# Optimization experiments

Hardware: AMD Instinct MI355X
Metric: run time of the kernel (lower is better)

The kernel has to match this reference:

```python
import jax, jax.numpy as jnp
import numpy as np

B, C_IN, N, K, UP = 4, 128, 1024, 9, 4
EPS_BN = 1e-5


def _grid():
    # gen_grid(4): num_x=num_y=2, linspace(-0.2,0.2,2) -> (4,2)
    g = jnp.linspace(-0.2, 0.2, 2)
    x, y = jnp.meshgrid(g, g, indexing='ij')
    return jnp.stack([x, y], axis=-1).reshape(-1, 2)


def _knn(x, k, dilation):
    # x: (B,C,N). L2-normalize features, matrix pairwise dist, top-k, dilated select.
    nrm = jnp.sqrt(jnp.sum(x * x, axis=1, keepdims=True))
    xn = x / jnp.maximum(nrm, 1e-12)
    xt = xn.transpose(0, 2, 1)                      # (B,N,C)
    sq = jnp.sum(xt * xt, axis=-1)                  # (B,N)
    dist = sq[:, :, None] - 2.0 * jnp.einsum('bnc,bmc->bnm', xt, xt) + sq[:, None, :]
    _, idx = jax.lax.top_k(-dist, k * dilation)     # k*d nearest (incl. self)
    return idx[:, :, ::dilation]                    # (B,N,k)


def _bn(x, g, b, axes):
    # training-mode batchnorm over given axes, channel axis = 1
    m = jnp.mean(x, axis=axes, keepdims=True)
    v = jnp.mean((x - m) ** 2, axis=axes, keepdims=True)
    sh = [1] * x.ndim
    sh[1] = -1
    return (x - m) * jax.lax.rsqrt(v + EPS_BN) * g.reshape(sh) + b.reshape(sh)


def _edge_conv(x, k, dil, W, g, b):
    # DGCNN edge conv: gather neighbors, [x_i, x_j-x_i], 1x1 conv, BN, relu, max over k
    idx = _knn(x, k, dil)                                        # (B,N,k)
    x_j = jax.vmap(lambda xx, ii: xx[:, ii])(x, idx)             # (B,C,N,k)
    x_i = jnp.broadcast_to(x[..., None], x_j.shape)
    feat = jnp.concatenate([x_i, x_j - x_i], axis=1)             # (B,2C,N,k)
    out = jnp.einsum('oc,bcnk->bonk', W, feat)
    out = jax.nn.relu(_bn(out, g, b, (0, 2, 3)))
    return jnp.max(out, axis=-1)                                 # (B,Cout,N)


def _conv1d(x, W, b):
    return jnp.einsum('oc,bcn->bon', W, x) + b[None, :, None]


def _atten(x, Wf, bf, gf, bef, Wg, bg, gg, beg, Wh, bh, gh, beh, gamma):
    # attention_unit / RA_Layer1 math (C=130)
    f = jax.nn.relu(_bn(_conv1d(x, Wf, bf), gf, bef, (0, 2)))    # (B,C/4,M)
    g_ = jax.nn.relu(_bn(_conv1d(x, Wg, bg), gg, beg, (0, 2)))
    h = jax.nn.relu(_bn(_conv1d(x, Wh, bh), gh, beh, (0, 2)))    # (B,C,M)
    s = jnp.einsum('bcn,bcm->bnm', g_, f)                        # g^T @ f: (B,M,M)
    beta = jax.nn.softmax(s, axis=2)
    o = jnp.einsum('bcn,bnm->bcm', h, beta)                      # h @ beta
    return gamma * o + x


def _forward(inp, Wa, gna, bta, Wb, gnb, btb, Wf, bf, gf, bef, Wg, bg, gg, beg,
             Wh, bh, gh, beh, gamma, W1, b1, W2, b2):
    x1 = _edge_conv(inp, K, 1, Wa, gna, bta)                     # (B,256,N)
    x2 = _edge_conv(inp, K, 2, Wb, gnb, btb)                     # (B,256,N)
    x = jnp.concatenate([x1, x2], axis=1)                        # (B,512,N)
    net = x.transpose(0, 2, 1).reshape(B, N * UP, 128)           # (B,4N,128)
    grid = jnp.repeat(_grid(), N, axis=0)                        # (4N,2)
    grid = jnp.broadcast_to(grid[None], (B, N * UP, 2)).astype(net.dtype)
    net = jnp.concatenate([net, grid], axis=2).transpose(0, 2, 1)  # (B,130,4N)
    net = _atten(net, Wf, bf, gf, bef, Wg, bg, gg, beg, Wh, bh, gh, beh, gamma)
    net = jax.nn.relu(_conv1d(net, W1, b1))                      # 130->256
    net = jax.nn.relu(_conv1d(net, W2, b2))                      # 256->128
    return net                                                   # (B,128,4N)


def setup_inputs() -> dict:
    key = jax.random.key(0)
    ks = jax.random.split(key, 24)
    rn = lambda k, sh, s=0.05: jax.random.normal(k, sh, jnp.float32) * s
    d = {
        'inp': jax.random.normal(ks[0], (B, C_IN, N), jnp.float32),
        'Wa': rn(ks[1], (256, 256)), 'gna': 1.0 + rn(ks[2], (256,)), 'bta': rn(ks[3], (256,)),
        'Wb': rn(ks[4], (256, 256)), 'gnb': 1.0 + rn(ks[5], (256,)), 'btb': rn(ks[6], (256,)),
        'Wf': rn(ks[7], (32, 130)), 'bf': rn(ks[8], (32,)), 'gf': 1.0 + rn(ks[9], (32,)), 'bef': rn(ks[9], (32,)),
        'Wg': rn(ks[10], (32, 130)), 'bg': rn(ks[11], (32,)), 'gg': 1.0 + rn(ks[12], (32,)), 'beg': rn(ks[12], (32,)),
        'Wh': rn(ks[13], (130, 130)), 'bh': rn(ks[14], (130,)), 'gh': 1.0 + rn(ks[15], (130,)), 'beh': rn(ks[15], (130,)),
        'gamma': rn(ks[16], (), 1.0),
        'W1': rn(ks[17], (256, 130)), 'b1': rn(ks[18], (256,)),
        'W2': rn(ks[19], (128, 256)), 'b2': rn(ks[20], (128,)),
    }
    return d


def reference(inp, Wa, gna, bta, Wb, gnb, btb, Wf, bf, gf, bef, Wg, bg, gg, beg,
              Wh, bh, gh, beh, gamma, W1, b1, W2, b2):
    return _forward(inp, Wa, gna, bta, Wb, gnb, btb, Wf, bf, gf, bef, Wg, bg, gg, beg,
                    Wh, bh, gh, beh, gamma, W1, b1, W2, b2)
```

## Files before the change

kernel.cpp:

```cpp
#include <hip/hip_runtime.h>

namespace {
constexpr int NB = 4;
constexpr int CI = 128;
constexpr int NP = 1024;
constexpr int MM = 4096;
constexpr float EPSBN = 1e-5f;
constexpr float LOG2E = 1.4426950408889634f;

constexpr size_t OPS_SH = 2162688;
constexpr size_t OFF_OP   = 0;
constexpr size_t OFF_DIST = 0;
constexpr size_t OFF_PM   = 0;
constexpr size_t OFF_QM   = 2097152;
constexpr size_t OFF_HRAW = 0;
constexpr size_t OFF_FGRAW= 2359296;
constexpr size_t OFF_Y1   = 0;
constexpr size_t OFF_FGT  = 6488064;
constexpr size_t OFF_HB   = 7012352;
constexpr size_t OFF_A16  = 6488064;
constexpr size_t OFF_X16  = 8192000;
constexpr size_t OFF_LSE  = 9502720;
constexpr size_t OFF_LSEP = 9519104;
constexpr size_t OFF_STATS= 9650176;
constexpr size_t OFF_ABE  = 9715712;
constexpr size_t OFF_ABFG = 9716736;
constexpr size_t OFF_ABH  = 9716864;
constexpr size_t OFF_FGP  = 9717376;
constexpr size_t OFF_BIAS = 9725568;
constexpr size_t OFF_W16  = 9726208;
constexpr size_t OFF_KNN  = 9779712;
constexpr size_t OFF_XN   = 9853440;
constexpr size_t OFF_SQ   = 10377728;
constexpr size_t OFF_XR   = 10381824;
constexpr size_t OFF_WPQ  = 10643968;
constexpr size_t W16_FG = 0;
constexpr size_t W16_H  = 10240;
constexpr size_t W16_C1 = 33280;
constexpr size_t W16_C2 = 74240;
constexpr size_t B_FG = 0, B_H = 64, B_C1 = 208, B_C2 = 464;
}

typedef __attribute__((ext_vector_type(8))) short short8;
typedef __attribute__((ext_vector_type(4))) float f32x4;
#define MFMA16(A, B, C) __builtin_amdgcn_mfma_f32_16x16x32_bf16(A, B, C, 0, 0, 0)

__device__ inline unsigned short f2bf(float x) {
  unsigned int u = __float_as_uint(x);
  unsigned int r = u + 0x7fff + ((u >> 16) & 1);
  return (unsigned short)(r >> 16);
}
__device__ inline float bf2f(unsigned short s) {
  return __uint_as_float(((unsigned int)s) << 16);
}
__device__ inline unsigned cvtpk(float lo, float hi) {
  unsigned r;
  asm("v_cvt_pk_bf16_f32 %0, %1, %2" : "=v"(r) : "v"(lo), "v"(hi));
  return r;
}

__global__ __launch_bounds__(256) void k_prep(const float* __restrict__ Wf, const float* __restrict__ Wg,
                                              const float* __restrict__ Wh, const float* __restrict__ W1,
                                              const float* __restrict__ W2, const float* __restrict__ bf,
                                              const float* __restrict__ bg, const float* __restrict__ bh,
                                              const float* __restrict__ b1, const float* __restrict__ b2,
                                              unsigned short* __restrict__ W16, float* __restrict__ BIAS) {
  int i = blockIdx.x * 256 + threadIdx.x;
  if (i < 107008) {
    float v = 0.f;
    if (i < 10240) { int o = i / 160, c = i % 160; if (c < 130) v = (o < 32) ? Wf[o * 130 + c] : Wg[(o - 32) * 130 + c]; }
    else if (i < 33280) { int r = i - 10240; int o = r / 160, c = r % 160; if (o < 130 && c < 130) v = Wh[o * 130 + c]; }
    else if (i < 74240) { int r = i - 33280; int o = r / 160, c = r % 160; if (c < 130) v = W1[o * 130 + c]; }
    else { int r = i - 74240; int o = r / 256, c = r % 256; v = W2[o * 256 + c]; }
    W16[i] = f2bf(v);
  } else if (i < 107648) {
    int j = i - 107008; float v = 0.f;
    if (j < 64) v = (j < 32) ? bf[j] : bg[j - 32];
    else if (j < 208) { int c = j - 64; if (c < 130) v = bh[c]; }
    else if (j < 464) v = b1[j - 208];
    else if (j < 592) v = b2[j - 464];
    BIAS[j] = v;
  }
}

__global__ __launch_bounds__(256) void k_prep2(const float* __restrict__ Wa, const float* __restrict__ Wb,
                                               unsigned short* __restrict__ WPQ) {
  int i = blockIdx.x * 256 + threadIdx.x;
  int e = i >> 16;
  int rem = i & 65535;
  int pq = rem >> 15;
  int rr = rem & 32767;
  int o = rr >> 7, c = rr & 127;
  const float* W = e ? Wb : Wa;
  float w1 = W[o * 256 + c], w2 = W[o * 256 + 128 + c];
  float v = pq ? w2 : (w1 - w2);
  WPQ[i] = f2bf(v);
}

__global__ __launch_bounds__(256) void k_norm(const float* __restrict__ x,
                                              float* __restrict__ xn,
                                              unsigned short* __restrict__ XR,
                                              float* __restrict__ sq) {
  int t = blockIdx.x * 256 + threadIdx.x;
  int b = t >> 10, n = t & 1023;
  const float* xb = x + (size_t)b * CI * NP + n;
  float ss = 0.f;
  #pragma unroll 4
  for (int c = 0; c < CI; ++c) { float v = xb[(size_t)c * NP]; ss += v * v; }
  float inv = 1.f / fmaxf(sqrtf(ss), 1e-12f);
  float* xo = xn + (size_t)b * CI * NP + n;
  float s2 = 0.f;
  for (int c0 = 0; c0 < 128; c0 += 8) {
    unsigned rw[4];
    #pragma unroll
    for (int j = 0; j < 4; ++j) {
      float va = xb[(size_t)(c0 + 2 * j) * NP];
      float vb = xb[(size_t)(c0 + 2 * j + 1) * NP];
      float na = va * inv, nb = vb * inv;
      s2 += na * na + nb * nb;
      xo[(size_t)(c0 + 2 * j) * NP] = na;
      xo[(size_t)(c0 + 2 * j + 1) * NP] = nb;
      rw[j] = (unsigned)f2bf(va) | ((unsigned)f2bf(vb) << 16);
    }
    uint4 r4 = {rw[0], rw[1], rw[2], rw[3]};
    *(uint4*)&XR[(size_t)t * 128 + c0] = r4;
  }
  sq[t] = s2;
}

__global__ __launch_bounds__(256) void k_dist(const float* __restrict__ xn,
                                              const float* __restrict__ sq,
                                              float* __restrict__ dist) {
  __shared__ float As[32][68], Bs[32][68];
  int t = threadIdx.x;
  int m0 = blockIdx.x * 64, n0 = blockIdx.y * 64, b = blockIdx.z;
  int mg = t & 15, ng = t >> 4;
  float acc[16];
  #pragma unroll
  for (int i = 0; i < 16; ++i) acc[i] = 0.f;
  for (int cc = 0; cc < 128; cc += 32) {
    __syncthreads();
    for (int idx = t; idx < 2048; idx += 256) {
      int c = idx >> 6, j = idx & 63;
      As[c][j] = xn[((size_t)b * CI + cc + c) * NP + n0 + j];
      Bs[c][j] = xn[((size_t)b * CI + cc + c) * NP + m0 + j];
    }
    __syncthreads();
    #pragma unroll
    for (int c = 0; c < 32; ++c) {
      float4 avv = *(const float4*)&As[c][ng * 4];
      float4 bvv = *(const float4*)&Bs[c][mg * 4];
      float a[4] = {avv.x, avv.y, avv.z, avv.w};
      float bb[4] = {bvv.x, bvv.y, bvv.z, bvv.w};
      #pragma unroll
      for (int i = 0; i < 4; ++i)
        #pragma unroll
        for (int j = 0; j < 4; ++j) acc[i * 4 + j] += a[i] * bb[j];
    }
  }
  #pragma unroll
  for (int i = 0; i < 4; ++i) {
    int n = n0 + ng * 4 + i;
    float sn = sq[b * NP + n];
    float4 r;
    r.x = sn + sq[b * NP + m0 + mg * 4 + 0] - 2.f * acc[i * 4 + 0];
    r.y = sn + sq[b * NP + m0 + mg * 4 + 1] - 2.f * acc[i * 4 + 1];
    r.z = sn + sq[b * NP + m0 + mg * 4 + 2] - 2.f * acc[i * 4 + 2];
    r.w = sn + sq[b * NP + m0 + mg * 4 + 3] - 2.f * acc[i * 4 + 3];
    *(float4*)&dist[((size_t)b * NP + n) * NP + m0 + mg * 4] = r;
  }
}

__global__ __launch_bounds__(64) void k_knn(const float* __restrict__ dist,
                                            int* __restrict__ knn) {
  int row = blockIdx.x;
  int l = threadIdx.x;
  const float* dr = dist + (size_t)row * NP;
  float d[16];
  #pragma unroll
  for (int i = 0; i < 16; ++i) d[i] = dr[l + 64 * i];
  for (int s = 0; s < 18; ++s) {
    float best = __builtin_inff(); int bslot = -1;
    #pragma unroll
    for (int i = 0; i < 16; ++i) if (d[i] < best) { best = d[i]; bslot = i; }
    int bidx = (bslot >= 0) ? (l + 64 * bslot) : 0x7fffffff;
    float bd = best; int bi = bidx;
    #pragma unroll
    for (int off = 32; off > 0; off >>= 1) {
      float od = __shfl_xor(bd, off);
      int   oi = __shfl_xor(bi, off);
      if (od < bd || (od == bd && oi < bi)) { bd = od; bi = oi; }
    }
    if (l == 0) knn[row * 18 + s] = bi;
    if ((bi & 63) == l) d[bi >> 6] = __builtin_inff();
  }
}

__global__ __launch_bounds__(256) void k_pqm(const unsigned short* __restrict__ XR,
                                             const unsigned short* __restrict__ WPQ,
                                             float* __restrict__ Pm,
                                             float* __restrict__ Qm) {
  int t = threadIdx.x; int w = t >> 6; int l = t & 63;
  int lm = l & 15, g = l >> 4;
  int nt = blockIdx.x, oq = blockIdx.y, z = blockIdx.z;
  int e = z >> 2, b = z & 3;
  int srow = nt * 64 + w * 16 + lm;
  const unsigned short* sp = XR + ((size_t)b * 1024 + srow) * 128 + 8 * g;
  const unsigned short* wpp = WPQ + ((size_t)(e * 2 + 0) * 256 + oq * 64 + lm) * 128 + 8 * g;
  const unsigned short* wqq = WPQ + ((size_t)(e * 2 + 1) * 256 + oq * 64 + lm) * 128 + 8 * g;
  f32x4 accp[4], accq[4];
  #pragma unroll
  for (int i = 0; i < 4; ++i) { accp[i] = {0.f, 0.f, 0.f, 0.f}; accq[i] = {0.f, 0.f, 0.f, 0.f}; }
  #pragma unroll
  for (int cc = 0; cc < 4; ++cc) {
    short8 bfr = *(const short8*)(sp + cc * 32);
    #pragma unroll
    for (int ct = 0; ct < 4; ++ct) {
      short8 ap = *(const short8*)(wpp + (size_t)ct * 16 * 128 + cc * 32);
      accp[ct] = MFMA16(ap, bfr, accp[ct]);
      short8 aq = *(const short8*)(wqq + (size_t)ct * 16 * 128 + cc * 32);
      accq[ct] = MFMA16(aq, bfr, accq[ct]);
    }
  }
  int eb = e * 4 + b;
  #pragma unroll
  for (int ct = 0; ct < 4; ++ct) {
    int o0 = oq * 64 + ct * 16 + 4 * g;
    float4 rp = {accp[ct][0], accp[ct][1], accp[ct][2], accp[ct][3]};
    float4 rq = {accq[ct][0], accq[ct][1], accq[ct][2], accq[ct][3]};
    *(float4*)&Pm[((size_t)eb * 1024 + srow) * 256 + o0] = rp;
    *(float4*)&Qm[((size_t)eb * 1024 + srow) * 256 + o0] = rq;
  }
}

__global__ __launch_bounds__(256) void k_edge_stats(const float* __restrict__ Pm,
                                                    const float* __restrict__ Qm,
                                                    const int* __restrict__ knn,
                                                    float* __restrict__ stats) {
  int o = threadIdx.x;
  int chunk = blockIdx.x, b = blockIdx.y, e = blockIdx.z;
  int eb = e * 4 + b;
  float s = 0.f, s2 = 0.f;
  for (int nn = 0; nn < 64; ++nn) {
    int n = chunk * 64 + nn;
    float p = Pm[((size_t)eb * 1024 + n) * 256 + o];
    const int* kn = knn + (b * 1024 + n) * 18;
    #pragma unroll
    for (int kk = 0; kk < 9; ++kk) {
      int j = kn[e ? 2 * kk : kk];
      float v = p + Qm[((size_t)eb * 1024 + j) * 256 + o];
      s += v; s2 += v * v;
    }
  }
  size_t idx = ((((size_t)e * 4 + b) * 16 + chunk) * 256 + o) * 2;
  stats[idx] = s; stats[idx + 1] = s2;
}

__global__ __launch_bounds__(256) void k_edge_fin(const float* __restrict__ stats,
                                                  const float* __restrict__ gna, const float* __restrict__ bta,
                                                  const float* __restrict__ gnb, const float* __restrict__ btb,
                                                  float* __restrict__ ab) {
  int i = blockIdx.x * 256 + threadIdx.x;
  if (i >= 512) return;
  int e = i >> 8, o = i & 255;
  float s = 0.f, s2 = 0.f;
  for (int b = 0; b < 4; ++b)
    for (int ch = 0; ch < 16; ++ch) {
      size_t idx = ((((size_t)e * 4 + b) * 16 + ch) * 256 + o) * 2;
      s += stats[idx]; s2 += stats[idx + 1];
    }
  float cnt = 4.0f * 1024.0f * 9.0f;
  float mean = s / cnt;
  float var = s2 / cnt - mean * mean;
  float g = e ? gnb[o] : gna[o];
  float bt = e ? btb[o] : bta[o];
  float alpha = g * rsqrtf(var + EPSBN);
  ab[i * 2] = alpha; ab[i * 2 + 1] = bt - mean * alpha;
}

__global__ __launch_bounds__(256) void k_edge_apply(const float* __restrict__ Pm,
                                                    const float* __restrict__ Qm,
                                                    const int* __restrict__ knn,
                                                    const float* __restrict__ ab,
                                                    unsigned short* __restrict__ X16) {
  __shared__ int knl[18];
  int t = threadIdx.x;
  int n = blockIdx.x, b = blockIdx.y;
  if (t < 18) knl[t] = knn[(b * 1024 + n) * 18 + t];
  __syncthreads();
  int e = t >> 7, oo = t & 127;
  int eb = e * 4 + b;
  const float* Pr = Pm + ((size_t)eb * 1024 + n) * 256;
  const float* Qb = Qm + (size_t)eb * 1024 * 256;
  float p0 = Pr[oo], p1 = Pr[oo + 128];
  float a0 = ab[(e * 256 + oo) * 2], be0 = ab[(e * 256 + oo) * 2 + 1];
  float a1 = ab[(e * 256 + oo + 128) * 2], be1 = ab[(e * 256 + oo + 128) * 2 + 1];
  float mx0 = -__builtin_inff(), mx1 = -__builtin_inff();
  #pragma unroll
  for (int kk = 0; kk < 9; ++kk) {
    int j = knl[e ? 2 * kk : kk];
    const float* Qr = Qb + (size_t)j * 256;
    mx0 = fmaxf(mx0, fmaf(a0, p0 + Qr[oo], be0));
    mx1 = fmaxf(mx1, fmaf(a1, p1 + Qr[oo + 128], be1));
  }
  int u0 = e << 1, u1 = (e << 1) | 1;
  X16[((size_t)b * MM + 4 * n + u0) * 160 + oo] = f2bf(fmaxf(mx0, 0.f));
  X16[((size_t)b * MM + 4 * n + u1) * 160 + oo] = f2bf(fmaxf(mx1, 0.f));
  if (t < 128) {
    int u = t >> 5, c = 128 + (t & 31);
    int gr = n >> 8;
    float v = (c == 128) ? ((gr < 2) ? -0.2f : 0.2f) : (c == 129) ? ((gr & 1) ? 0.2f : -0.2f) : 0.f;
    X16[((size_t)b * MM + 4 * n + u) * 160 + c] = f2bf(v);
  }
}

template <int KSTEPS, int CTPER, int OUTMODE, bool RELU>
__global__ __launch_bounds__(256) void k_convm(const unsigned short* __restrict__ src,
                                               const unsigned short* __restrict__ W16,
                                               const float* __restrict__ bias,
                                               float* __restrict__ dstF,
                                               unsigned short* __restrict__ dstB,
                                               int outld, int rows) {
  constexpr int LD = KSTEPS * 32;
  int t = threadIdx.x; int w = t >> 6; int l = t & 63;
  int lm = l & 15, g = l >> 4;
  int b = blockIdx.z; int ct0 = blockIdx.y * CTPER;
  int srow = blockIdx.x * 64 + w * 16 + lm;
  const unsigned short* sp = src + ((size_t)b * MM + srow) * LD + 8 * g;
  const unsigned short* wp = W16 + ((size_t)ct0 * 16 + lm) * LD + 8 * g;
  f32x4 acc[CTPER];
  #pragma unroll
  for (int i = 0; i < CTPER; ++i) acc[i] = {0.f, 0.f, 0.f, 0.f};
  #pragma unroll
  for (int cc = 0; cc < KSTEPS; ++cc) {
    short8 bfr = *(const short8*)(sp + cc * 32);
    #pragma unroll
    for (int ct = 0; ct < CTPER; ++ct) {
      short8 af = *(const short8*)(wp + (size_t)ct * 16 * LD + cc * 32);
      acc[ct] = MFMA16(af, bfr, acc[ct]);
    }
  }
  #pragma unroll
  for (int ct = 0; ct < CTPER; ++ct) {
    int o0 = (ct0 + ct) * 16 + 4 * g;
    float4 bv = *(const float4*)&bias[o0];
    float v[4] = {acc[ct][0] + bv.x, acc[ct][1] + bv.y, acc[ct][2] + bv.z, acc[ct][3] + bv.w};
    if (RELU) { v[0] = fmaxf(v[0], 0.f); v[1] = fmaxf(v[1], 0.f); v[2] = fmaxf(v[2], 0.f); v[3] = fmaxf(v[3], 0.f); }
    if (OUTMODE == 0) {
      float4 r = {v[0], v[1], v[2], v[3]};
      *(float4*)&dstF[((size_t)b * MM + srow) * outld + o0] = r;
    } else if (OUTMODE == 1) {
      uint2 pk;
      pk.x = cvtpk(v[0], v[1]);
      pk.y = cvtpk(v[2], v[3]);
      *(uint2*)&dstB[((size_t)b * MM + srow) * outld + o0] = pk;
    } else {
      #pragma unroll
      for (int r = 0; r < 4; ++r)
        dstF[((size_t)b * rows + o0 + r) * MM + srow] = v[r];
    }
  }
}

__global__ __launch_bounds__(256) void k_fgstats(const float* __restrict__ FGraw,
                                                 float* __restrict__ FGP) {
  __shared__ float red[4][64][2];
  int t = threadIdx.x; int c = t & 63, rq = t >> 6;
  int blk = blockIdx.x;
  float s = 0.f, s2 = 0.f;
  for (int k = 0; k < 64; ++k) {
    int r = blk * 256 + rq + 4 * k;
    float v = FGraw[(size_t)r * 64 + c];
    s += v; s2 += v * v;
  }
  red[rq][c][0] = s; red[rq][c][1] = s2;
  __syncthreads();
  if (t < 64) {
    float a = 0.f, a2 = 0.f;
    #pragma unroll
    for (int q = 0; q < 4; ++q) { a += red[q][t][0]; a2 += red[q][t][1]; }
    FGP[((size_t)blk * 64 + t) * 2] = a; FGP[((size_t)blk * 64 + t) * 2 + 1] = a2;
  }
}

__global__ __launch_bounds__(64) void k_fgfin(const float* __restrict__ FGP,
                                              const float* __restrict__ gf, const float* __restrict__ bef,
                                              const float* __restrict__ gg, const float* __restrict__ beg,
                                              float* __restrict__ ab) {
  int c = threadIdx.x;
  float s = 0.f, s2 = 0.f;
  for (int blk = 0; blk < 64; ++blk) { s += FGP[((size_t)blk * 64 + c) * 2]; s2 += FGP[((size_t)blk * 64 + c) * 2 + 1]; }
  float cnt = 16384.f;
  float mean = s / cnt, var = s2 / cnt - mean * mean;
  float gv = (c < 32) ? gf[c] : gg[c - 32];
  float bv = (c < 32) ? bef[c] : beg[c - 32];
  float alpha = gv * rsqrtf(var + EPSBN);
  ab[c * 2] = alpha; ab[c * 2 + 1] = bv - mean * alpha;
}

__global__ __launch_bounds__(256) void k_bnstats(const float* __restrict__ src,
                                                 const float* __restrict__ g,
                                                 const float* __restrict__ be,
                                                 float* __restrict__ ab, int ldC) {
  int o = blockIdx.x;
  int t = threadIdx.x;
  float s = 0.f, s2 = 0.f;
  for (int b = 0; b < NB; ++b) {
    const float* r = src + ((size_t)b * ldC + o) * MM;
    for (int m = t; m < MM; m += 256) { float v = r[m]; s += v; s2 += v * v; }
  }
  __shared__ float rs[256], rs2[256];
  rs[t] = s; rs2[t] = s2;
  __syncthreads();
  for (int off = 128; off > 0; off >>= 1) {
    if (t < off) { rs[t] += rs[t + off]; rs2[t] += rs2[t + off]; }
    __syncthreads();
  }
  if (t == 0) {
    float cnt = 16384.0f;
    float mean = rs[0] / cnt, var = rs2[0] / cnt - mean * mean;
    float alpha = g[o] * rsqrtf(var + EPSBN);
    ab[o * 2] = alpha; ab[o * 2 + 1] = be[o] - mean * alpha;
  }
}

__global__ __launch_bounds__(256) void k_cvtFG(const float* __restrict__ FGraw,
                                               const float* __restrict__ ab,
                                               unsigned short* __restrict__ FGT) {
  int i = blockIdx.x * 256 + threadIdx.x;
  int row = i >> 3, c0 = (i & 7) * 8;
  float sc = (c0 < 32) ? LOG2E : 1.0f;
  float vv[8];
  float4 u0 = *(const float4*)&FGraw[(size_t)row * 64 + c0];
  float4 u1 = *(const float4*)&FGraw[(size_t)row * 64 + c0 + 4];
  vv[0] = u0.x; vv[1] = u0.y; vv[2] = u0.z; vv[3] = u0.w;
  vv[4] = u1.x; vv[5] = u1.y; vv[6] = u1.z; vv[7] = u1.w;
  uint4 pk;
  unsigned pw[4];
  #pragma unroll
  for (int h = 0; h < 4; ++h) {
    int c = c0 + 2 * h;
    float a0 = ab[c * 2] * sc, b0 = ab[c * 2 + 1] * sc;
    float a1 = ab[(c + 1) * 2] * sc, b1 = ab[(c + 1) * 2 + 1] * sc;
    float x0 = fmaxf(fmaf(a0, vv[2 * h], b0), 0.f);
    float x1 = fmaxf(fmaf(a1, vv[2 * h + 1], b1), 0.f);
    pw[h] = cvtpk(x0, x1);
  }
  pk.x = pw[0]; pk.y = pw[1]; pk.z = pw[2]; pk.w = pw[3];
  *(uint4*)&FGT[(size_t)row * 64 + c0] = pk;
}

__global__ __launch_bounds__(256) void k_cvtH(const float* __restrict__ src,
                                              const float* __restrict__ ab,
                                              unsigned short* __restrict__ dst) {
  int i = blockIdx.x * 256 + threadIdx.x;
  int m4 = i & 1023; int c = (i >> 10) % 144; int b = i / (144 * 1024);
  ushort4 ov = {0, 0, 0, 0};
  if (c < 130) {
    float4 v = *(const float4*)&src[((size_t)b * 144 + c) * MM + m4 * 4];
    float a = ab[c * 2], be = ab[c * 2 + 1];
    ov.x = f2bf(fmaxf(fmaf(a, v.x, be), 0.f));
    ov.y = f2bf(fmaxf(fmaf(a, v.y, be), 0.f));
    ov.z = f2bf(fmaxf(fmaf(a, v.z, be), 0.f));
    ov.w = f2bf(fmaxf(fmaf(a, v.w, be), 0.f));
  }
  *(ushort4*)&dst[((size_t)b * 144 + c) * MM + m4 * 4] = ov;
}

__global__ __launch_bounds__(256) void k_zlse(const unsigned short* __restrict__ FGT,
                                              float* __restrict__ LSEP) {
  int t = threadIdx.x; int w = t >> 6; int l = t & 63;
  int b = blockIdx.z; int ms = blockIdx.y;
  int n0 = blockIdx.x * 64 + w * 16;
  int lm = l & 15, g = l >> 4;
  f32x4 z4 = {0.f, 0.f, 0.f, 0.f};
  short8 af = *(const short8*)&FGT[((size_t)b * MM + n0 + lm) * 64 + 32 + 8 * g];
  float rm[4], zz[4];
  #pragma unroll
  for (int r = 0; r < 4; ++r) { rm[r] = -__builtin_inff(); zz[r] = 0.f; }
  for (int it = 0; it < 16; ++it) {
    int m0 = ms * 1024 + it * 64;
    short8 bfr[4];
    #pragma unroll
    for (int mi = 0; mi < 4; ++mi)
      bfr[mi] = *(const short8*)&FGT[((size_t)b * MM + m0 + mi * 16 + lm) * 64 + 8 * g];
    f32x4 d[4];
    #pragma unroll
    for (int mi = 0; mi < 4; ++mi) d[mi] = MFMA16(af, bfr[mi], z4);
    #pragma unroll
    for (int r = 0; r < 4; ++r) {
      float tm = fmaxf(fmaxf(d[0][r], d[1][r]), fmaxf(d[2][r], d[3][r]));
      float nm = fmaxf(rm[r], tm);
      zz[r] = zz[r] * exp2f(rm[r] - nm)
            + exp2f(d[0][r] - nm) + exp2f(d[1][r] - nm)
            + exp2f(d[2][r] - nm) + exp2f(d[3][r] - nm);
      rm[r] = nm;
    }
  }
  #pragma unroll
  for (int off = 1; off < 16; off <<= 1) {
    #pragma unroll
    for (int r = 0; r < 4; ++r) {
      float om = __shfl_xor(rm[r], off);
      float oz = __shfl_xor(zz[r], off);
      float nm = fmaxf(rm[r], om);
      zz[r] = zz[r] * exp2f(rm[r] - nm) + oz * exp2f(om - nm);
      rm[r] = nm;
    }
  }
  if (lm == 0) {
    #pragma unroll
    for (int r = 0; r < 4; ++r) {
      int n = n0 + 4 * g + r;
      size_t idx = ((size_t)ms * 16384 + (size_t)b * MM + n) * 2;
      LSEP[idx] = rm[r]; LSEP[idx + 1] = zz[r];
    }
  }
}

__global__ __launch_bounds__(256) void k_lsered(const float* __restrict__ LSEP,
                                                float* __restrict__ LSE) {
  int bn = blockIdx.x * 256 + threadIdx.x;
  float rm = -__builtin_inff(), zz = 0.f;
  #pragma unroll
  for (int ms = 0; ms < 4; ++ms) {
    float m = LSEP[((size_t)ms * 16384 + bn) * 2];
    float z = LSEP[((size_t)ms * 16384 + bn) * 2 + 1];
    float nm = fmaxf(rm, m);
    zz = zz * exp2f(rm - nm) + z * exp2f(m - nm);
    rm = nm;
  }
  LSE[bn] = rm + log2f(zz);
}

__global__ __launch_bounds__(256) void k_omfma(const unsigned short* __restrict__ FGT,
                                               const unsigned short* __restrict__ HB,
                                               const float* __restrict__ LSE,
                                               unsigned short* __restrict__ Opart) {
  int t = threadIdx.x; int w = t >> 6; int l = t & 63;
  int b = blockIdx.y; int split = blockIdx.z;
  int lm = l & 15, g = l >> 4;
  int mcol0 = blockIdx.x * 128 + w * 32 + lm;
  int mcol1 = mcol0 + 16;
  f32x4 z4 = {0.f, 0.f, 0.f, 0.f};
  short8 Ff0 = *(const short8*)&FGT[((size_t)b * MM + mcol0) * 64 + 8 * g];
  short8 Ff1 = *(const short8*)&FGT[((size_t)b * MM + mcol1) * 64 + 8 * g];
  f32x4 acc0[9], acc1[9];
  #pragma unroll
  for (int ct = 0; ct < 9; ++ct) { acc0[ct] = z4; acc1[ct] = z4; }
  const int nchunks = (split < 2) ? 22 : 21;
  const int startc = split * 21 + ((split < 2) ? split : 2);
  const int start = startc * 32;
  const int end = start + nchunks * 32;
  const unsigned short* gptr = FGT + ((size_t)b * MM + lm) * 64 + 32 + 8 * g;
  const unsigned short* hbase = HB + ((size_t)b * 144 + lm) * MM + 8 * g;
  const float* lbase = LSE + (size_t)b * MM + 4 * g;
  int src01 = lm + 16 * (2 * (g & 1));
  int src23 = src01 + 16;
  bool hi = g >= 2;

  short8 a0 = *(const short8*)(gptr + (size_t)start * 64);
  short8 a1 = *(const short8*)(gptr + (size_t)(start + 16) * 64);
  float4 l0 = *(const float4*)(lbase + start);
  float4 l1 = *(const float4*)(lbase + start + 16);

  for (int n0 = start; n0 < end; n0 += 32) {
    const unsigned short* hp = hbase + n0;
    short8 hf[9];
    #pragma unroll
    for (int ct = 0; ct < 9; ++ct) hf[ct] = *(const short8*)(hp + (size_t)ct * 16 * MM);
    f32x4 s00 = MFMA16(a0, Ff0, z4);
    f32x4 s10 = MFMA16(a1, Ff0, z4);
    f32x4 s01 = MFMA16(a0, Ff1, z4);
    f32x4 s11 = MFMA16(a1, Ff1, z4);
    int nn = (n0 + 32 < end) ? (n0 + 32) : start;
    short8 na0 = *(const short8*)(gptr + (size_t)nn * 64);
    short8 na1 = *(const short8*)(gptr + (size_t)(nn + 16) * 64);
    float4 nl0 = *(const float4*)(lbase + nn);
    float4 nl1 = *(const float4*)(lbase + nn + 16);
    float le0[4] = {l0.x, l0.y, l0.z, l0.w};
    float le1[4] = {l1.x, l1.y, l1.z, l1.w};
    unsigned pk00[2], pk10[2], pk01[2], pk11[2];
    #pragma unroll
    for (int h2 = 0; h2 < 2; ++h2) {
      float e00a = exp2f(s00[2 * h2] - le0[2 * h2]);
      float e00b = exp2f(s00[2 * h2 + 1] - le0[2 * h2 + 1]);
      float e10a = exp2f(s10[2 * h2] - le1[2 * h2]);
      float e10b = exp2f(s10[2 * h2 + 1] - le1[2 * h2 + 1]);
      float e01a = exp2f(s01[2 * h2] - le0[2 * h2]);
      float e01b = exp2f(s01[2 * h2 + 1] - le0[2 * h2 + 1]);
      float e11a = exp2f(s11[2 * h2] - le1[2 * h2]);
      float e11b = exp2f(s11[2 * h2 + 1] - le1[2 * h2 + 1]);
      pk00[h2] = cvtpk(e00a, e00b);
      pk10[h2] = cvtpk(e10a, e10b);
      pk01[h2] = cvtpk(e01a, e01b);
      pk11[h2] = cvtpk(e11a, e11b);
    }
    a0 = na0; a1 = na1; l0 = nl0; l1 = nl1;
    unsigned a0w = (unsigned)__shfl((int)pk00[0], src01);
    unsigned b0w = (unsigned)__shfl((int)pk10[0], src01);
    unsigned a1w = (unsigned)__shfl((int)pk00[1], src01);
    unsigned b1w = (unsigned)__shfl((int)pk10[1], src01);
    unsigned a2w = (unsigned)__shfl((int)pk00[0], src23);
    unsigned b2w = (unsigned)__shfl((int)pk10[0], src23);
    unsigned a3w = (unsigned)__shfl((int)pk00[1], src23);
    unsigned b3w = (unsigned)__shfl((int)pk10[1], src23);
    union { unsigned u[4]; short8 s; } bu0;
    bu0.u[0] = hi ? b0w : a0w; bu0.u[1] = hi ? b1w : a1w;
    bu0.u[2] = hi ? b2w : a2w; bu0.u[3] = hi ? b3w : a3w;
    short8 bfrag0 = bu0.s;
    unsigned c0w = (unsigned)__shfl((int)pk01[0], src01);
    unsigned d0w = (unsigned)__shfl((int)pk11[0], src01);
    unsigned c1w = (unsigned)__shfl((int)pk01[1], src01);
    unsigned d1w = (unsigned)__shfl((int)pk11[1], src01);
    unsigned c2w = (unsigned)__shfl((int)pk01[0], src23);
    unsigned d2w = (unsigned)__shfl((int)pk11[0], src23);
    unsigned c3w = (unsigned)__shfl((int)pk01[1], src23);
    unsigned d3w = (unsigned)__shfl((int)pk11[1], src23);
    union { unsigned u[4]; short8 s; } bu1;
    bu1.u[0] = hi ? d0w : c0w; bu1.u[1] = hi ? d1w : c1w;
    bu1.u[2] = hi ? d2w : c2w; bu1.u[3] = hi ? d3w : c3w;
    short8 bfrag1 = bu1.s;
    #pragma unroll
    for (int ct = 0; ct < 9; ++ct) {
      acc0[ct] = MFMA16(hf[ct], bfrag0, acc0[ct]);
      acc1[ct] = MFMA16(hf[ct], bfrag1, acc1[ct]);
    }
  }
  unsigned short* op0 = Opart + (size_t)split * OPS_SH + ((size_t)b * MM + mcol0) * 132;
  unsigned short* op1 = Opart + (size_t)split * OPS_SH + ((size_t)b * MM + mcol1) * 132;
  #pragma unroll
  for (int ct = 0; ct < 9; ++ct) {
    int c0 = ct * 16 + 4 * g;
    if (c0 < 132) {
      uint2 p0, p1;
      p0.x = cvtpk(acc0[ct][0], acc0[ct][1]);
      p0.y = cvtpk(acc0[ct][2], acc0[ct][3]);
      p1.x = cvtpk(acc1[ct][0], acc1[ct][1]);
      p1.y = cvtpk(acc1[ct][2], acc1[ct][3]);
      *(uint2*)&op0[c0] = p0;
      *(uint2*)&op1[c0] = p1;
    }
  }
}

__global__ __launch_bounds__(256) void k_ored(const unsigned short* __restrict__ Op,
                                              const unsigned short* __restrict__ X16,
                                              const float* __restrict__ gma,
                                              unsigned short* __restrict__ A16) {
  int i = blockIdx.x * 256 + threadIdx.x;
  int row = i / 20, c8 = i % 20;
  int c0 = c8 * 8;
  unsigned short* ap = A16 + (size_t)row * 160 + c0;
  if (c0 >= 136) {
    uint4 z = {0, 0, 0, 0};
    *(uint4*)ap = z;
    return;
  }
  float gm = gma[0];
  float ov[8] = {0.f, 0.f, 0.f, 0.f, 0.f, 0.f, 0.f, 0.f};
  #pragma unroll
  for (int s = 0; s < 6; ++s) {
    const unsigned short* base = Op + (size_t)s * OPS_SH + (size_t)row * 132 + c0;
    uint2 u = *(const uint2*)base;
    ov[0] += bf2f((unsigned short)(u.x & 0xffff));
    ov[1] += bf2f((unsigned short)(u.x >> 16));
    ov[2] += bf2f((unsigned short)(u.y & 0xffff));
    ov[3] += bf2f((unsigned short)(u.y >> 16));
    if (c0 + 4 < 132) {
      uint2 v = *(const uint2*)(base + 4);
      ov[4] += bf2f((unsigned short)(v.x & 0xffff));
      ov[5] += bf2f((unsigned short)(v.x >> 16));
      ov[6] += bf2f((unsigned short)(v.y & 0xffff));
      ov[7] += bf2f((unsigned short)(v.y >> 16));
    }
  }
  short8 xv = *(const short8*)(X16 + (size_t)row * 160 + c0);
  unsigned pw[4];
  #pragma unroll
  for (int h = 0; h < 4; ++h) {
    int ca = c0 + 2 * h, cb = c0 + 2 * h + 1;
    float xa = bf2f((unsigned short)xv[2 * h]);
    float xb = bf2f((unsigned short)xv[2 * h + 1]);
    float va = (ca < 132) ? (gm * ov[2 * h] + xa) : 0.f;
    float vb = (cb < 132) ? (gm * ov[2 * h + 1] + xb) : 0.f;
    pw[h] = (unsigned)f2bf(va) | ((unsigned)f2bf(vb) << 16);
  }
  uint4 pk = {pw[0], pw[1], pw[2], pw[3]};
  *(uint4*)ap = pk;
}

extern "C" void kernel_launch(void* const* d_in, const int* in_sizes, int n_in,
                              void* d_out, int out_size, void* d_ws, size_t ws_size,
                              hipStream_t stream) {
  const float* inp = (const float*)d_in[0];
  const float* Wa  = (const float*)d_in[1];
  const float* gna = (const float*)d_in[2];
  const float* bta = (const float*)d_in[3];
  const float* Wb  = (const float*)d_in[4];
  const float* gnb = (const float*)d_in[5];
  const float* btb = (const float*)d_in[6];
  const float* Wf  = (const float*)d_in[7];
  const float* bf  = (const float*)d_in[8];
  const float* gf  = (const float*)d_in[9];
  const float* bef = (const float*)d_in[10];
  const float* Wg  = (const float*)d_in[11];
  const float* bg  = (const float*)d_in[12];
  const float* gg  = (const float*)d_in[13];
  const float* beg = (const float*)d_in[14];
  const float* Wh  = (const float*)d_in[15];
  const float* bh  = (const float*)d_in[16];
  const float* gh  = (const float*)d_in[17];
  const float* beh = (const float*)d_in[18];
  const float* gamma = (const float*)d_in[19];
  const float* W1  = (const float*)d_in[20];
  const float* b1  = (const float*)d_in[21];
  const float* W2  = (const float*)d_in[22];
  const float* b2  = (const float*)d_in[23];
  float* out = (float*)d_out;

  float* ws = (float*)d_ws;
  float* DIST = ws + OFF_DIST;
  float* PM   = ws + OFF_PM;
  float* QM   = ws + OFF_QM;
  float* HRAW = ws + OFF_HRAW;
  float* FGRAW= ws + OFF_FGRAW;
  unsigned short* OP16 = (unsigned short*)(ws + OFF_OP);
  unsigned short* FGT = (unsigned short*)(ws + OFF_FGT);
  unsigned short* HBB = (unsigned short*)(ws + OFF_HB);
  unsigned short* A16 = (unsigned short*)(ws + OFF_A16);
  unsigned short* X16 = (unsigned short*)(ws + OFF_X16);
  unsigned short* Y1  = (unsigned short*)(ws + OFF_Y1);
  float* LSEB = ws + OFF_LSE;
  float* LSEP = ws + OFF_LSEP;
  float* STATS= ws + OFF_STATS;
  float* ABE  = ws + OFF_ABE;
  float* ABFG = ws + OFF_ABFG;
  float* ABH  = ws + OFF_ABH;
  float* FGP  = ws + OFF_FGP;
  float* BIAS = ws + OFF_BIAS;
  unsigned short* W16 = (unsigned short*)(ws + OFF_W16);
  int*   KNNI = (int*)(ws + OFF_KNN);
  float* XN   = ws + OFF_XN;
  unsigned short* XR = (unsigned short*)(ws + OFF_XR);
  unsigned short* WPQ = (unsigned short*)(ws + OFF_WPQ);
  float* SQ   = ws + OFF_SQ;

  k_prep<<<421, 256, 0, stream>>>(Wf, Wg, Wh, W1, W2, bf, bg, bh, b1, b2, W16, BIAS);
  k_prep2<<<512, 256, 0, stream>>>(Wa, Wb, WPQ);
  k_norm<<<16, 256, 0, stream>>>(inp, XN, XR, SQ);
  k_dist<<<dim3(16, 16, 4), 256, 0, stream>>>(XN, SQ, DIST);
  k_knn<<<4096, 64, 0, stream>>>(DIST, KNNI);
  k_pqm<<<dim3(16, 4, 8), 256, 0, stream>>>(XR, WPQ, PM, QM);
  k_edge_stats<<<dim3(16, 4, 2), 256, 0, stream>>>(PM, QM, KNNI, STATS);
  k_edge_fin<<<2, 256, 0, stream>>>(STATS, gna, bta, gnb, btb, ABE);
  k_edge_apply<<<dim3(1024, 4), 256, 0, stream>>>(PM, QM, KNNI, ABE, X16);
  k_convm<5, 2, 0, false><<<dim3(64, 2, 4), 256, 0, stream>>>(X16, W16 + W16_FG, BIAS + B_FG, FGRAW, nullptr, 64, 0);
  k_convm<5, 3, 2, false><<<dim3(64, 3, 4), 256, 0, stream>>>(X16, W16 + W16_H, BIAS + B_H, HRAW, nullptr, 0, 144);
  k_fgstats<<<64, 256, 0, stream>>>(FGRAW, FGP);
  k_fgfin<<<1, 64, 0, stream>>>(FGP, gf, bef, gg, beg, ABFG);
  k_bnstats<<<130, 256, 0, stream>>>(HRAW, gh, beh, ABH, 144);
  k_cvtFG<<<512, 256, 0, stream>>>(FGRAW, ABFG, FGT);
  k_cvtH<<<2304, 256, 0, stream>>>(HRAW, ABH, HBB);
  k_zlse<<<dim3(64, 4, 4), 256, 0, stream>>>(FGT, LSEP);
  k_lsered<<<64, 256, 0, stream>>>(LSEP, LSEB);
  k_omfma<<<dim3(32, 4, 6), 256, 0, stream>>>(FGT, HBB, LSEB, OP16);
  k_ored<<<1280, 256, 0, stream>>>(OP16, X16, gamma, A16);
  k_convm<5, 8, 1, true><<<dim3(64, 2, 4), 256, 0, stream>>>(A16, W16 + W16_C1, BIAS + B_C1, nullptr, Y1, 256, 0);
  k_convm<8, 4, 2, true><<<dim3(64, 2, 4), 256, 0, stream>>>(Y1, W16 + W16_C2, BIAS + B_C2, out, nullptr, 0, 128);
}
```

Before: 352.3 us.

## Store raw F/G/H conv outputs in bf16, merge prep kernels, deepen omfma prefetch

The F/G and H 1x1 conv outputs are now written in bf16 rather than fp32. BN statistics and the normalize/ReLU apply step read those bf16 buffers, and H is normalized in place. This halves intermediate memory traffic, at the cost of computing BN statistics on bf16-rounded values. The two weight-prep kernels are merged into one launch. The attention MFMA loop is software-pipelined two iterations ahead so the score MFMAs for the next tile overlap with the current softmax and accumulation.

```diff
diff --git a/kernel.cpp b/kernel.cpp
--- a/kernel.cpp
+++ b/kernel.cpp
@@ -13,8 +13,7 @@
 constexpr size_t OFF_DIST = 0;
 constexpr size_t OFF_PM   = 0;
 constexpr size_t OFF_QM   = 2097152;
-constexpr size_t OFF_HRAW = 0;
-constexpr size_t OFF_FGRAW= 2359296;
+constexpr size_t OFF_FGR  = 2359296;
 constexpr size_t OFF_Y1   = 0;
 constexpr size_t OFF_FGT  = 6488064;
 constexpr size_t OFF_HB   = 7012352;
@@ -64,7 +63,9 @@
                                               const float* __restrict__ W2, const float* __restrict__ bf,
                                               const float* __restrict__ bg, const float* __restrict__ bh,
                                               const float* __restrict__ b1, const float* __restrict__ b2,
-                                              unsigned short* __restrict__ W16, float* __restrict__ BIAS) {
+                                              const float* __restrict__ Wa, const float* __restrict__ Wb,
+                                              unsigned short* __restrict__ W16, float* __restrict__ BIAS,
+                                              unsigned short* __restrict__ WPQ) {
   int i = blockIdx.x * 256 + threadIdx.x;
   if (i < 107008) {
     float v = 0.f;
@@ -80,21 +81,18 @@
     else if (j < 464) v = b1[j - 208];
     else if (j < 592) v = b2[j - 464];
     BIAS[j] = v;
-  }
-}
-
-__global__ __launch_bounds__(256) void k_prep2(const float* __restrict__ Wa, const float* __restrict__ Wb,
-                                               unsigned short* __restrict__ WPQ) {
-  int i = blockIdx.x * 256 + threadIdx.x;
-  int e = i >> 16;
-  int rem = i & 65535;
-  int pq = rem >> 15;
-  int rr = rem & 32767;
-  int o = rr >> 7, c = rr & 127;
-  const float* W = e ? Wb : Wa;
-  float w1 = W[o * 256 + c], w2 = W[o * 256 + 128 + c];
-  float v = pq ? w2 : (w1 - w2);
-  WPQ[i] = f2bf(v);
+  } else if (i < 238720) {
+    int j = i - 107648;
+    int e = j >> 16;
+    int rem = j & 65535;
+    int pq = rem >> 15;
+    int rr = rem & 32767;
+    int o = rr >> 7, c = rr & 127;
+    const float* W = e ? Wb : Wa;
+    float w1 = W[o * 256 + c], w2 = W[o * 256 + 128 + c];
+    float v = pq ? w2 : (w1 - w2);
+    WPQ[j] = f2bf(v);
+  }
 }
 
 __global__ __launch_bounds__(256) void k_norm(const float* __restrict__ x,
@@ -354,15 +352,19 @@
       pk.x = cvtpk(v[0], v[1]);
       pk.y = cvtpk(v[2], v[3]);
       *(uint2*)&dstB[((size_t)b * MM + srow) * outld + o0] = pk;
+    } else if (OUTMODE == 2) {
+      #pragma unroll
+      for (int r = 0; r < 4; ++r)
+        dstF[((size_t)b * rows + o0 + r) * MM + srow] = v[r];
     } else {
       #pragma unroll
       for (int r = 0; r < 4; ++r)
-        dstF[((size_t)b * rows + o0 + r) * MM + srow] = v[r];
-    }
-  }
-}
-
-__global__ __launch_bounds__(256) void k_fgstats(const float* __restrict__ FGraw,
+        dstB[((size_t)b * rows + o0 + r) * MM + srow] = f2bf(v[r]);
+    }
+  }
+}
+
+__global__ __launch_bounds__(256) void k_fgstats(const unsigned short* __restrict__ FGR,
                                                  float* __restrict__ FGP) {
   __shared__ float red[4][64][2];
   int t = threadIdx.x; int c = t & 63, rq = t >> 6;
@@ -370,7 +372,7 @@
   float s = 0.f, s2 = 0.f;
   for (int k = 0; k < 64; ++k) {
     int r = blk * 256 + rq + 4 * k;
-    float v = FGraw[(size_t)r * 64 + c];
+    float v = bf2f(FGR[(size_t)r * 64 + c]);
     s += v; s2 += v * v;
   }
   red[rq][c][0] = s; red[rq][c][1] = s2;
@@ -398,16 +400,49 @@
   ab[c * 2] = alpha; ab[c * 2 + 1] = bv - mean * alpha;
 }
 
-__global__ __launch_bounds__(256) void k_bnstats(const float* __restrict__ src,
-                                                 const float* __restrict__ g,
-                                                 const float* __restrict__ be,
-                                                 float* __restrict__ ab, int ldC) {
+__global__ __launch_bounds__(256) void k_applyFG(const unsigned short* __restrict__ FGR,
+                                                 const float* __restrict__ ab,
+                                                 unsigned short* __restrict__ FGT) {
+  int i = blockIdx.x * 256 + threadIdx.x;
+  int row = i >> 3, c0 = (i & 7) * 8;
+  float sc = (c0 < 32) ? LOG2E : 1.0f;
+  uint4 u = *(const uint4*)&FGR[(size_t)row * 64 + c0];
+  unsigned uw[4] = {u.x, u.y, u.z, u.w};
+  unsigned pw[4];
+  #pragma unroll
+  for (int h = 0; h < 4; ++h) {
+    int c = c0 + 2 * h;
+    float a0 = ab[c * 2] * sc, b0 = ab[c * 2 + 1] * sc;
+    float a1 = ab[(c + 1) * 2] * sc, b1 = ab[(c + 1) * 2 + 1] * sc;
+    float v0 = bf2f((unsigned short)(uw[h] & 0xffff));
+    float v1 = bf2f((unsigned short)(uw[h] >> 16));
+    float x0 = fmaxf(fmaf(a0, v0, b0), 0.f);
+    float x1 = fmaxf(fmaf(a1, v1, b1), 0.f);
+    pw[h] = cvtpk(x0, x1);
+  }
+  uint4 pk = {pw[0], pw[1], pw[2], pw[3]};
+  *(uint4*)&FGT[(size_t)row * 64 + c0] = pk;
+}
+
+__global__ __launch_bounds__(256) void k_bnstatsH(const unsigned short* __restrict__ HBR,
+                                                  const float* __restrict__ g,
+                                                  const float* __restrict__ be,
+                                                  float* __restrict__ ab) {
   int o = blockIdx.x;
   int t = threadIdx.x;
   float s = 0.f, s2 = 0.f;
   for (int b = 0; b < NB; ++b) {
-    const float* r = src + ((size_t)b * ldC + o) * MM;
-    for (int m = t; m < MM; m += 256) { float v = r[m]; s += v; s2 += v * v; }
+    const unsigned short* r = HBR + ((size_t)b * 144 + o) * MM;
+    for (int m = t * 8; m < MM; m += 2048) {
+      uint4 u = *(const uint4*)&r[m];
+      unsigned uw[4] = {u.x, u.y, u.z, u.w};
+      #pragma unroll
+      for (int h = 0; h < 4; ++h) {
+        float v0 = bf2f((unsigned short)(uw[h] & 0xffff));
+        float v1 = bf2f((unsigned short)(uw[h] >> 16));
+        s += v0 + v1; s2 += v0 * v0 + v1 * v1;
+      }
+    }
   }
   __shared__ float rs[256], rs2[256];
   rs[t] = s; rs2[t] = s2;
@@ -424,47 +459,30 @@
   }
 }
 
-__global__ __launch_bounds__(256) void k_cvtFG(const float* __restrict__ FGraw,
-                                               const float* __restrict__ ab,
-                                               unsigned short* __restrict__ FGT) {
+__global__ __launch_bounds__(256) void k_applyH(unsigned short* __restrict__ HBR,
+                                                const float* __restrict__ ab) {
   int i = blockIdx.x * 256 + threadIdx.x;
-  int row = i >> 3, c0 = (i & 7) * 8;
-  float sc = (c0 < 32) ? LOG2E : 1.0f;
-  float vv[8];
-  float4 u0 = *(const float4*)&FGraw[(size_t)row * 64 + c0];
-  float4 u1 = *(const float4*)&FGraw[(size_t)row * 64 + c0 + 4];
-  vv[0] = u0.x; vv[1] = u0.y; vv[2] = u0.z; vv[3] = u0.w;
-  vv[4] = u1.x; vv[5] = u1.y; vv[6] = u1.z; vv[7] = u1.w;
-  uint4 pk;
+  int c = (i >> 9) % 144;
+  unsigned short* p = HBR + (size_t)i * 8;
+  if (c >= 130) {
+    uint4 z = {0, 0, 0, 0};
+    *(uint4*)p = z;
+    return;
+  }
+  float a = ab[c * 2], be = ab[c * 2 + 1];
+  uint4 u = *(const uint4*)p;
+  unsigned uw[4] = {u.x, u.y, u.z, u.w};
   unsigned pw[4];
   #pragma unroll
   for (int h = 0; h < 4; ++h) {
-    int c = c0 + 2 * h;
-    float a0 = ab[c * 2] * sc, b0 = ab[c * 2 + 1] * sc;
-    float a1 = ab[(c + 1) * 2] * sc, b1 = ab[(c + 1) * 2 + 1] * sc;
-    float x0 = fmaxf(fmaf(a0, vv[2 * h], b0), 0.f);
-    float x1 = fmaxf(fmaf(a1, vv[2 * h + 1], b1), 0.f);
+    float v0 = bf2f((unsigned short)(uw[h] & 0xffff));
+    float v1 = bf2f((unsigned short)(uw[h] >> 16));
+    float x0 = fmaxf(fmaf(a, v0, be), 0.f);
+    float x1 = fmaxf(fmaf(a, v1, be), 0.f);
     pw[h] = cvtpk(x0, x1);
   }
-  pk.x = pw[0]; pk.y = pw[1]; pk.z = pw[2]; pk.w = pw[3];
-  *(uint4*)&FGT[(size_t)row * 64 + c0] = pk;
-}
-
-__global__ __launch_bounds__(256) void k_cvtH(const float* __restrict__ src,
-                                              const float* __restrict__ ab,
-                                              unsigned short* __restrict__ dst) {
-  int i = blockIdx.x * 256 + threadIdx.x;
-  int m4 = i & 1023; int c = (i >> 10) % 144; int b = i / (144 * 1024);
-  ushort4 ov = {0, 0, 0, 0};
-  if (c < 130) {
-    float4 v = *(const float4*)&src[((size_t)b * 144 + c) * MM + m4 * 4];
-    float a = ab[c * 2], be = ab[c * 2 + 1];
-    ov.x = f2bf(fmaxf(fmaf(a, v.x, be), 0.f));
-    ov.y = f2bf(fmaxf(fmaf(a, v.y, be), 0.f));
-    ov.z = f2bf(fmaxf(fmaf(a, v.z, be), 0.f));
-    ov.w = f2bf(fmaxf(fmaf(a, v.w, be), 0.f));
-  }
-  *(ushort4*)&dst[((size_t)b * 144 + c) * MM + m4 * 4] = ov;
+  uint4 pk = {pw[0], pw[1], pw[2], pw[3]};
+  *(uint4*)p = pk;
 }
 
 __global__ __launch_bounds__(256) void k_zlse(const unsigned short* __restrict__ FGT,
@@ -551,7 +569,8 @@
   const int nchunks = (split < 2) ? 22 : 21;
   const int startc = split * 21 + ((split < 2) ? split : 2);
   const int start = startc * 32;
-  const int end = start + nchunks * 32;
+  const int span = nchunks * 32;
+  const int end = start + span;
   const unsigned short* gptr = FGT + ((size_t)b * MM + lm) * 64 + 32 + 8 * g;
   const unsigned short* hbase = HB + ((size_t)b * 144 + lm) * MM + 8 * g;
   const float* lbase = LSE + (size_t)b * MM + 4 * g;
@@ -561,25 +580,30 @@
 
   short8 a0 = *(const short8*)(gptr + (size_t)start * 64);
   short8 a1 = *(const short8*)(gptr + (size_t)(start + 16) * 64);
-  float4 l0 = *(const float4*)(lbase + start);
-  float4 l1 = *(const float4*)(lbase + start + 16);
+  float4 l0c = *(const float4*)(lbase + start);
+  float4 l1c = *(const float4*)(lbase + start + 16);
+  f32x4 s00 = MFMA16(a0, Ff0, z4);
+  f32x4 s10 = MFMA16(a1, Ff0, z4);
+  f32x4 s01 = MFMA16(a0, Ff1, z4);
+  f32x4 s11 = MFMA16(a1, Ff1, z4);
+  int n1 = start + 32; if (n1 >= end) n1 = start;
+  short8 a0n = *(const short8*)(gptr + (size_t)n1 * 64);
+  short8 a1n = *(const short8*)(gptr + (size_t)(n1 + 16) * 64);
+  float4 l0n = *(const float4*)(lbase + n1);
+  float4 l1n = *(const float4*)(lbase + n1 + 16);
 
   for (int n0 = start; n0 < end; n0 += 32) {
     const unsigned short* hp = hbase + n0;
     short8 hf[9];
     #pragma unroll
     for (int ct = 0; ct < 9; ++ct) hf[ct] = *(const short8*)(hp + (size_t)ct * 16 * MM);
-    f32x4 s00 = MFMA16(a0, Ff0, z4);
-    f32x4 s10 = MFMA16(a1, Ff0, z4);
-    f32x4 s01 = MFMA16(a0, Ff1, z4);
-    f32x4 s11 = MFMA16(a1, Ff1, z4);
-    int nn = (n0 + 32 < end) ? (n0 + 32) : start;
-    short8 na0 = *(const short8*)(gptr + (size_t)nn * 64);
-    short8 na1 = *(const short8*)(gptr + (size_t)(nn + 16) * 64);
-    float4 nl0 = *(const float4*)(lbase + nn);
-    float4 nl1 = *(const float4*)(lbase + nn + 16);
-    float le0[4] = {l0.x, l0.y, l0.z, l0.w};
-    float le1[4] = {l1.x, l1.y, l1.z, l1.w};
+    int n2 = n0 + 64; if (n2 >= end) n2 -= span;
+    short8 a0f = *(const short8*)(gptr + (size_t)n2 * 64);
+    short8 a1f = *(const short8*)(gptr + (size_t)(n2 + 16) * 64);
+    float4 l0f = *(const float4*)(lbase + n2);
+    float4 l1f = *(const float4*)(lbase + n2 + 16);
+    float le0[4] = {l0c.x, l0c.y, l0c.z, l0c.w};
+    float le1[4] = {l1c.x, l1c.y, l1c.z, l1c.w};
     unsigned pk00[2], pk10[2], pk01[2], pk11[2];
     #pragma unroll
     for (int h2 = 0; h2 < 2; ++h2) {
@@ -596,7 +620,10 @@
       pk01[h2] = cvtpk(e01a, e01b);
       pk11[h2] = cvtpk(e11a, e11b);
     }
-    a0 = na0; a1 = na1; l0 = nl0; l1 = nl1;
+    f32x4 t00 = MFMA16(a0n, Ff0, z4);
+    f32x4 t10 = MFMA16(a1n, Ff0, z4);
+    f32x4 t01 = MFMA16(a0n, Ff1, z4);
+    f32x4 t11 = MFMA16(a1n, Ff1, z4);
     unsigned a0w = (unsigned)__shfl((int)pk00[0], src01);
     unsigned b0w = (unsigned)__shfl((int)pk10[0], src01);
     unsigned a1w = (unsigned)__shfl((int)pk00[1], src01);
@@ -626,6 +653,9 @@
       acc0[ct] = MFMA16(hf[ct], bfrag0, acc0[ct]);
       acc1[ct] = MFMA16(hf[ct], bfrag1, acc1[ct]);
     }
+    s00 = t00; s10 = t10; s01 = t01; s11 = t11;
+    l0c = l0n; l1c = l1n; l0n = l0f; l1n = l1f;
+    a0n = a0f; a1n = a1f;
   }
   unsigned short* op0 = Opart + (size_t)split * OPS_SH + ((size_t)b * MM + mcol0) * 132;
   unsigned short* op1 = Opart + (size_t)split * OPS_SH + ((size_t)b * MM + mcol1) * 132;
@@ -723,11 +753,10 @@
   float* DIST = ws + OFF_DIST;
   float* PM   = ws + OFF_PM;
   float* QM   = ws + OFF_QM;
-  float* HRAW = ws + OFF_HRAW;
-  float* FGRAW= ws + OFF_FGRAW;
+  unsigned short* FGR = (unsigned short*)(ws + OFF_FGR);
   unsigned short* OP16 = (unsigned short*)(ws + OFF_OP);
   unsigned short* FGT = (unsigned short*)(ws + OFF_FGT);
-  unsigned short* HBB = (unsigned short*)(ws + OFF_HB);
+  unsigned short* HBR = (unsigned short*)(ws + OFF_HB);
   unsigned short* A16 = (unsigned short*)(ws + OFF_A16);
   unsigned short* X16 = (unsigned short*)(ws + OFF_X16);
   unsigned short* Y1  = (unsigned short*)(ws + OFF_Y1);
@@ -746,8 +775,7 @@
   unsigned short* WPQ = (unsigned short*)(ws + OFF_WPQ);
   float* SQ   = ws + OFF_SQ;
 
-  k_prep<<<421, 256, 0, stream>>>(Wf, Wg, Wh, W1, W2, bf, bg, bh, b1, b2, W16, BIAS);
-  k_prep2<<<512, 256, 0, stream>>>(Wa, Wb, WPQ);
+  k_prep<<<933, 256, 0, stream>>>(Wf, Wg, Wh, W1, W2, bf, bg, bh, b1, b2, Wa, Wb, W16, BIAS, WPQ);
   k_norm<<<16, 256, 0, stream>>>(inp, XN, XR, SQ);
   k_dist<<<dim3(16, 16, 4), 256, 0, stream>>>(XN, SQ, DIST);
   k_knn<<<4096, 64, 0, stream>>>(DIST, KNNI);
@@ -755,16 +783,16 @@
   k_edge_stats<<<dim3(16, 4, 2), 256, 0, stream>>>(PM, QM, KNNI, STATS);
   k_edge_fin<<<2, 256, 0, stream>>>(STATS, gna, bta, gnb, btb, ABE);
   k_edge_apply<<<dim3(1024, 4), 256, 0, stream>>>(PM, QM, KNNI, ABE, X16);
-  k_convm<5, 2, 0, false><<<dim3(64, 2, 4), 256, 0, stream>>>(X16, W16 + W16_FG, BIAS + B_FG, FGRAW, nullptr, 64, 0);
-  k_convm<5, 3, 2, false><<<dim3(64, 3, 4), 256, 0, stream>>>(X16, W16 + W16_H, BIAS + B_H, HRAW, nullptr, 0, 144);
-  k_fgstats<<<64, 256, 0, stream>>>(FGRAW, FGP);
+  k_convm<5, 2, 1, false><<<dim3(64, 2, 4), 256, 0, stream>>>(X16, W16 + W16_FG, BIAS + B_FG, nullptr, FGR, 64, 0);
+  k_convm<5, 3, 3, false><<<dim3(64, 3, 4), 256, 0, stream>>>(X16, W16 + W16_H, BIAS + B_H, nullptr, HBR, 0, 144);
+  k_fgstats<<<64, 256, 0, stream>>>(FGR, FGP);
   k_fgfin<<<1, 64, 0, stream>>>(FGP, gf, bef, gg, beg, ABFG);
-  k_bnstats<<<130, 256, 0, stream>>>(HRAW, gh, beh, ABH, 144);
-  k_cvtFG<<<512, 256, 0, stream>>>(FGRAW, ABFG, FGT);
-  k_cvtH<<<2304, 256, 0, stream>>>(HRAW, ABH, HBB);
+  k_bnstatsH<<<130, 256, 0, stream>>>(HBR, gh, beh, ABH);
+  k_applyFG<<<512, 256, 0, stream>>>(FGR, ABFG, FGT);
+  k_applyH<<<1152, 256, 0, stream>>>(HBR, ABH);
   k_zlse<<<dim3(64, 4, 4), 256, 0, stream>>>(FGT, LSEP);
   k_lsered<<<64, 256, 0, stream>>>(LSEP, LSEB);
-  k_omfma<<<dim3(32, 4, 6), 256, 0, stream>>>(FGT, HBB, LSEB, OP16);
+  k_omfma<<<dim3(32, 4, 6), 256, 0, stream>>>(FGT, HBR, LSEB, OP16);
   k_ored<<<1280, 256, 0, stream>>>(OP16, X16, gamma, A16);
   k_convm<5, 8, 1, true><<<dim3(64, 2, 4), 256, 0, stream>>>(A16, W16 + W16_C1, BIAS + B_C1, nullptr, Y1, 256, 0);
   k_convm<8, 4, 2, true><<<dim3(64, 2, 4), 256, 0, stream>>>(Y1, W16 + W16_C2, BIAS + B_C2, out, nullptr, 0, 128);
```

Measured after the change: 338.1 us. 1.04x faster.
